# Performance work log

Measured on AMD Instinct MI355X. Metric: run time of the kernel, lower is better.

The kernel has to match this reference:

```python
import jax, jax.numpy as jnp
import numpy as np

N = 100000
H = 512
NUM_HEADS = 8
G = 512  # number of graphs (segments)


def seg_softmax(s, batch, num_segments):
    # numerically stable segment softmax (PyG-style, +1e-16 in denom)
    m = jax.ops.segment_max(s, batch, num_segments=num_segments)
    e = jnp.exp(s - m[batch])
    d = jax.ops.segment_sum(e, batch, num_segments=num_segments)
    return e / (d[batch] + 1e-16)


def setup_inputs() -> dict:
    key = jax.random.key(0)
    ks = jax.random.split(key, 12)
    s = 0.02
    x = jax.random.normal(ks[0], (N, H), dtype=jnp.float32)
    batch = jnp.sort(jax.random.randint(ks[1], (N,), 0, G)).astype(jnp.int64)
    # GlobalAttention.gate_nn: Linear(H, H//2) -> ReLU -> Linear(H//2, 1)
    ga_g_w1 = jax.random.normal(ks[2], (H, H // 2), dtype=jnp.float32) * s
    ga_g_b1 = jnp.zeros((H // 2,), dtype=jnp.float32)
    ga_g_w2 = jax.random.normal(ks[3], (H // 2, 1), dtype=jnp.float32) * s
    ga_g_b2 = jnp.zeros((1,), dtype=jnp.float32)
    # GlobalAttention.nn: Linear(H, H) -> ReLU
    ga_n_w = jax.random.normal(ks[4], (H, H), dtype=jnp.float32) * s
    ga_n_b = jnp.zeros((H,), dtype=jnp.float32)
    # outer gate_nn: Linear(H, H) -> ReLU -> (Dropout: identity in eval) -> Linear(H, NUM_HEADS)
    g_w1 = jax.random.normal(ks[5], (H, H), dtype=jnp.float32) * s
    g_b1 = jnp.zeros((H,), dtype=jnp.float32)
    g_w2 = jax.random.normal(ks[6], (H, NUM_HEADS), dtype=jnp.float32) * s
    g_b2 = jnp.zeros((NUM_HEADS,), dtype=jnp.float32)
    return dict(x=x, batch=batch,
                ga_g_w1=ga_g_w1, ga_g_b1=ga_g_b1, ga_g_w2=ga_g_w2, ga_g_b2=ga_g_b2,
                ga_n_w=ga_n_w, ga_n_b=ga_n_b,
                g_w1=g_w1, g_b1=g_b1, g_w2=g_w2, g_b2=g_b2)


def reference(x, batch, ga_g_w1, ga_g_b1, ga_g_w2, ga_g_b2, ga_n_w, ga_n_b,
              g_w1, g_b1, g_w2, g_b2):
    # --- GlobalAttention pooling ---
    h = jax.nn.relu(x @ ga_g_w1 + ga_g_b1)          # (N, H//2)
    gate = (h @ ga_g_w2 + ga_g_b2)[:, 0]            # (N,)
    gate = seg_softmax(gate, batch, G)              # segment softmax per graph
    xt = jax.nn.relu(x @ ga_n_w + ga_n_b)           # (N, H)
    graph_embedding = jax.ops.segment_sum(gate[:, None] * xt, batch,
                                          num_segments=G)  # (G, H)
    # --- interpretable attention weights ---
    g = jax.nn.relu(x @ g_w1 + g_b1)                # (N, H); dropout = identity (eval)
    scores = (g @ g_w2 + g_b2).mean(axis=-1)        # (N,) mean over heads
    attention = seg_softmax(scores, batch, G)       # (N,)
    return graph_embedding, attention
```

## Files before the change

### kernel.cpp

```cpp
#include <hip/hip_runtime.h>

#define NN 100000
#define HH 512
#define GG 512
#define NPACK 1280
#define NSTRIP 80
#define SB 16384
#define XTROWS (NN + 128)

typedef unsigned short u16;
typedef unsigned int u32;
typedef __bf16 bf16x8 __attribute__((ext_vector_type(8)));
typedef unsigned short u16x8 __attribute__((ext_vector_type(8)));
typedef float f32x4 __attribute__((ext_vector_type(4)));
typedef __attribute__((address_space(1))) void gvoid_t;
typedef __attribute__((address_space(3))) void lvoid_t;

__device__ __forceinline__ u16 f2bf(float f) {
    unsigned u = __float_as_uint(f);
    unsigned r = u + 0x7FFFu + ((u >> 16) & 1u);
    return (u16)(r >> 16);
}
__device__ __forceinline__ float bf2f(u16 b) {
    return __uint_as_float(((unsigned)b) << 16);
}

__global__ void k_prep(const float* __restrict__ gw1, const float* __restrict__ gb1,
                       const float* __restrict__ gw2v,
                       const float* __restrict__ nw, const float* __restrict__ nb,
                       const float* __restrict__ aw1, const float* __restrict__ ab1,
                       const float* __restrict__ aw2, const int* __restrict__ batch,
                       u16* __restrict__ WT, float2* __restrict__ bwv,
                       int* __restrict__ starts) {
    int idx = blockIdx.x * blockDim.x + threadIdx.x;
    int stride = gridDim.x * blockDim.x;
    for (int i = idx; i < NPACK * 512; i += stride) {
        int n = i >> 9, k = i & 511;
        float v;
        if (n < 256)      v = gw1[k * 256 + n];
        else if (n < 768) v = nw[k * 512 + (n - 256)];
        else              v = aw1[k * 512 + (n - 768)];
        int s = n >> 4, nl = n & 15;
        int ck = k >> 3, k3 = k & 7;
        size_t byte = (size_t)s * SB + nl * 1024 + ((size_t)(ck ^ nl) << 4) + k3 * 2;
        *(u16*)((char*)WT + byte) = f2bf(v);
    }
    for (int n = idx; n < NPACK; n += stride) {
        float bi, wv;
        if (n < 256)      { bi = gb1[n];       wv = gw2v[n]; }
        else if (n < 768) { bi = nb[n - 256];  wv = 0.f; }
        else {
            bi = ab1[n - 768];
            float s = 0.f;
            for (int h = 0; h < 8; ++h) s += aw2[(n - 768) * 8 + h];
            wv = s * 0.125f;
        }
        bwv[n] = make_float2(bi, wv);
    }
    for (int g = idx; g <= GG; g += stride) {
        if (g == GG) { starts[GG] = NN; continue; }
        int lo = 0, hi = NN;
        while (lo < hi) { int mid = (lo + hi) >> 1; if (batch[mid] < g) lo = mid + 1; else hi = mid; }
        starts[g] = lo;
    }
}

__global__ __launch_bounds__(256, 2)
void k_gemm(const float* __restrict__ X, const u16* __restrict__ B,
            const float2* __restrict__ bwv,
            const float* __restrict__ gb2, const float* __restrict__ ab2,
            u16* __restrict__ xt, float* __restrict__ gs, float* __restrict__ as_) {
    __shared__ __align__(16) char ldsB[2 * SB];
    __shared__ __align__(8) float2 bwv_lds[NPACK];

    const int tid = threadIdx.x;
    const int lane = tid & 63;
    const int w = tid >> 6;
    const int m0 = blockIdx.x * 128;
    const int l16 = lane & 15, kq = lane >> 4;

#define STAGE(s, bsel) do {                                                          \
    const char* _src = (const char*)B + (size_t)(s) * SB + tid * 16;                 \
    char* _dst = ldsB + (bsel) * SB + tid * 16;                                      \
    _Pragma("unroll")                                                                \
    for (int _t = 0; _t < 4; ++_t)                                                   \
        __builtin_amdgcn_global_load_lds((gvoid_t*)(_src + _t * 4096),               \
                                         (lvoid_t*)(_dst + _t * 4096), 16, 0, 0);    \
} while (0)

    STAGE(0, 0);

    for (int t = tid; t < NPACK; t += 256) bwv_lds[t] = bwv[t];

    float b2 = gb2[0];
    float bb = 0.f;
#pragma unroll
    for (int h = 0; h < 8; ++h) bb += ab2[h];
    bb *= 0.125f;

    __syncthreads();

    bf16x8 a_reg[2][16];
#pragma unroll
    for (int i = 0; i < 2; ++i) {
        int row = m0 + w * 32 + i * 16 + l16;
        if (row >= NN) row = NN - 1;
        const float* xp = X + (size_t)row * 512 + kq * 8;
#pragma unroll
        for (int kt = 0; kt < 16; ++kt) {
            float4 f0 = *(const float4*)(xp + kt * 32);
            float4 f1 = *(const float4*)(xp + kt * 32 + 4);
            u16x8 u;
            u[0] = f2bf(f0.x); u[1] = f2bf(f0.y); u[2] = f2bf(f0.z); u[3] = f2bf(f0.w);
            u[4] = f2bf(f1.x); u[5] = f2bf(f1.y); u[6] = f2bf(f1.z); u[7] = f2bf(f1.w);
            a_reg[i][kt] = __builtin_bit_cast(bf16x8, u);
        }
    }

    float s_[2][4];
#pragma unroll
    for (int i = 0; i < 2; ++i)
#pragma unroll
        for (int r = 0; r < 4; ++r) s_[i][r] = 0.f;
    u32 stash[4];

    for (int nt = 0; nt < NSTRIP; ++nt) {
        const int cur = nt & 1;
        if (nt + 1 < NSTRIP) STAGE(nt + 1, cur ^ 1);

        if (nt == NSTRIP - 1)
            asm volatile("s_waitcnt vmcnt(0)" ::: "memory");
        else if (nt >= 18 && nt <= 48 && !(nt & 1))
            asm volatile("s_waitcnt vmcnt(12)" ::: "memory");
        else
            asm volatile("s_waitcnt vmcnt(4)" ::: "memory");
        __builtin_amdgcn_s_barrier();
        __builtin_amdgcn_sched_barrier(0);

        f32x4 acc[2];
        acc[0] = {0.f, 0.f, 0.f, 0.f};
        acc[1] = {0.f, 0.f, 0.f, 0.f};

        const char* bbase = ldsB + cur * SB + l16 * 1024;
        __builtin_amdgcn_s_setprio(1);
#pragma unroll
        for (int kt = 0; kt < 16; ++kt) {
            int off = ((kt * 4 + kq) ^ l16) << 4;
            bf16x8 b0 = *(const bf16x8*)(bbase + off);
            acc[0] = __builtin_amdgcn_mfma_f32_16x16x32_bf16(a_reg[0][kt], b0, acc[0], 0, 0, 0);
            acc[1] = __builtin_amdgcn_mfma_f32_16x16x32_bf16(a_reg[1][kt], b0, acc[1], 0, 0, 0);
        }
        __builtin_amdgcn_s_setprio(0);
        __builtin_amdgcn_s_barrier();

        float2 bw = bwv_lds[nt * 16 + l16];
        if (nt < 16) {
#pragma unroll
            for (int i = 0; i < 2; ++i)
#pragma unroll
                for (int r = 0; r < 4; ++r)
                    s_[i][r] += fmaxf(acc[i][r] + bw.x, 0.f) * bw.y;
            if (nt == 15) {
#pragma unroll
                for (int i = 0; i < 2; ++i)
#pragma unroll
                    for (int r = 0; r < 4; ++r) {
                        float pg = s_[i][r];
                        pg += __shfl_xor(pg, 1); pg += __shfl_xor(pg, 2);
                        pg += __shfl_xor(pg, 4); pg += __shfl_xor(pg, 8);
                        int rg = m0 + w * 32 + i * 16 + kq * 4 + r;
                        if (l16 == 0 && rg < NN) gs[rg] = pg + b2;
                        s_[i][r] = 0.f;
                    }
            }
        } else if (nt < 48) {
            const int sx = nt - 16;
            if (!(sx & 1)) {
#pragma unroll
                for (int i = 0; i < 2; ++i)
#pragma unroll
                    for (int rp = 0; rp < 2; ++rp) {
                        u32 lo = f2bf(fmaxf(acc[i][rp * 2]     + bw.x, 0.f));
                        u32 hi = f2bf(fmaxf(acc[i][rp * 2 + 1] + bw.x, 0.f));
                        stash[i * 2 + rp] = lo | (hi << 16);
                    }
            } else {
                const int s2 = sx >> 1;
#pragma unroll
                for (int i = 0; i < 2; ++i)
#pragma unroll
                    for (int r = 0; r < 4; ++r) {
                        int rg = m0 + w * 32 + i * 16 + kq * 4 + r;
                        ushort2 st;
                        st.x = (u16)(stash[i * 2 + (r >> 1)] >> ((r & 1) * 16));
                        st.y = f2bf(fmaxf(acc[i][r] + bw.x, 0.f));
                        *(ushort2*)(xt + (size_t)rg * 512 + s2 * 32 + l16 * 2) = st;
                    }
            }
        } else {
#pragma unroll
            for (int i = 0; i < 2; ++i)
#pragma unroll
                for (int r = 0; r < 4; ++r)
                    s_[i][r] += fmaxf(acc[i][r] + bw.x, 0.f) * bw.y;
        }
    }
#undef STAGE

#pragma unroll
    for (int i = 0; i < 2; ++i)
#pragma unroll
        for (int r = 0; r < 4; ++r) {
            float pa = s_[i][r];
            pa += __shfl_xor(pa, 1); pa += __shfl_xor(pa, 2);
            pa += __shfl_xor(pa, 4); pa += __shfl_xor(pa, 8);
            int rg = m0 + w * 32 + i * 16 + kq * 4 + r;
            if (l16 == 0 && rg < NN) as_[rg] = pa + bb;
        }
}

__global__ void k_seg(const float* __restrict__ gs, const float* __restrict__ as_,
                      const int* __restrict__ starts,
                      float* __restrict__ gate, float* __restrict__ attn) {
    int g = blockIdx.x;
    int s0 = starts[g], s1 = starts[g + 1];
    int tid = threadIdx.x, lane = tid & 63, w = tid >> 6;
    __shared__ float red[8];
    float lmg = -3.0e38f, lma = -3.0e38f;
    for (int i = s0 + tid; i < s1; i += 256) {
        lmg = fmaxf(lmg, gs[i]); lma = fmaxf(lma, as_[i]);
    }
    for (int o = 32; o; o >>= 1) {
        lmg = fmaxf(lmg, __shfl_xor(lmg, o));
        lma = fmaxf(lma, __shfl_xor(lma, o));
    }
    if (lane == 0) { red[w] = lmg; red[4 + w] = lma; }
    __syncthreads();
    float Mg = fmaxf(fmaxf(red[0], red[1]), fmaxf(red[2], red[3]));
    float Ma = fmaxf(fmaxf(red[4], red[5]), fmaxf(red[6], red[7]));
    __syncthreads();
    float sgv = 0.f, sav = 0.f;
    for (int i = s0 + tid; i < s1; i += 256) {
        sgv += expf(gs[i] - Mg); sav += expf(as_[i] - Ma);
    }
    for (int o = 32; o; o >>= 1) { sgv += __shfl_xor(sgv, o); sav += __shfl_xor(sav, o); }
    if (lane == 0) { red[w] = sgv; red[4 + w] = sav; }
    __syncthreads();
    float Dg = red[0] + red[1] + red[2] + red[3] + 1e-16f;
    float Da = red[4] + red[5] + red[6] + red[7] + 1e-16f;
    for (int i = s0 + tid; i < s1; i += 256) {
        gate[i] = expf(gs[i] - Mg) / Dg;
        attn[i] = expf(as_[i] - Ma) / Da;
    }
}

__global__ __launch_bounds__(256)
void k_emb(const u16* __restrict__ xt, const float* __restrict__ gate,
           const int* __restrict__ starts, float* __restrict__ out) {
    int g = blockIdx.x;
    int s0 = starts[g], s1 = starts[g + 1];
    int c2 = threadIdx.x;
    int col0 = (c2 >> 4) * 32 + (c2 & 15);
    float a0 = 0.f, a1 = 0.f;
    int n = s0;
    for (; n + 4 <= s1; n += 4) {
        ushort2 u0 = reinterpret_cast<const ushort2*>(xt + (size_t)(n + 0) * 512)[c2];
        ushort2 u1 = reinterpret_cast<const ushort2*>(xt + (size_t)(n + 1) * 512)[c2];
        ushort2 u2 = reinterpret_cast<const ushort2*>(xt + (size_t)(n + 2) * 512)[c2];
        ushort2 u3 = reinterpret_cast<const ushort2*>(xt + (size_t)(n + 3) * 512)[c2];
        float g0 = gate[n], g1 = gate[n + 1], g2 = gate[n + 2], g3 = gate[n + 3];
        a0 += g0 * bf2f(u0.x); a1 += g0 * bf2f(u0.y);
        a0 += g1 * bf2f(u1.x); a1 += g1 * bf2f(u1.y);
        a0 += g2 * bf2f(u2.x); a1 += g2 * bf2f(u2.y);
        a0 += g3 * bf2f(u3.x); a1 += g3 * bf2f(u3.y);
    }
    for (; n < s1; ++n) {
        float gn = gate[n];
        ushort2 u = reinterpret_cast<const ushort2*>(xt + (size_t)n * 512)[c2];
        a0 += gn * bf2f(u.x);
        a1 += gn * bf2f(u.y);
    }
    out[g * 512 + col0] = a0;
    out[g * 512 + col0 + 16] = a1;
}

extern "C" void kernel_launch(void* const* d_in, const int* in_sizes, int n_in,
                              void* d_out, int out_size, void* d_ws, size_t ws_size,
                              hipStream_t stream) {
    const float* x       = (const float*)d_in[0];
    const int*   batch   = (const int*)d_in[1];
    const float* ga_g_w1 = (const float*)d_in[2];
    const float* ga_g_b1 = (const float*)d_in[3];
    const float* ga_g_w2 = (const float*)d_in[4];
    const float* ga_g_b2 = (const float*)d_in[5];
    const float* ga_n_w  = (const float*)d_in[6];
    const float* ga_n_b  = (const float*)d_in[7];
    const float* g_w1    = (const float*)d_in[8];
    const float* g_b1    = (const float*)d_in[9];
    const float* g_w2    = (const float*)d_in[10];
    const float* g_b2    = (const float*)d_in[11];

    float* out_emb = (float*)d_out;
    float* out_att = out_emb + GG * HH;

    char* p = (char*)d_ws;
    size_t off = 0;
    auto alloc = [&](size_t bytes) -> char* {
        char* q = p + off;
        off += (bytes + 255) & ~(size_t)255;
        return q;
    };
    u16*    xt    = (u16*)   alloc((size_t)XTROWS * HH * 2);
    u16*    WT    = (u16*)   alloc((size_t)NPACK * 512 * 2);
    float2* bwv   = (float2*)alloc(NPACK * 8);
    float*  gs    = (float*) alloc((size_t)NN * 4);
    float*  as_   = (float*) alloc((size_t)NN * 4);
    float*  gate  = (float*) alloc((size_t)NN * 4);
    int*    starts= (int*)   alloc((GG + 1) * 4);

    k_prep<<<2560, 256, 0, stream>>>(ga_g_w1, ga_g_b1, ga_g_w2, ga_n_w, ga_n_b,
                                     g_w1, g_b1, g_w2, batch, WT, bwv, starts);
    k_gemm<<<782, 256, 0, stream>>>(x, WT, bwv, ga_g_b2, g_b2, xt, gs, as_);
    k_seg<<<GG, 256, 0, stream>>>(gs, as_, starts, gate, out_att);
    k_emb<<<GG, 256, 0, stream>>>(xt, gate, starts, out_emb);
}
```

Baseline: 522.2 us.

## Widen GEMM strips to 32 columns, fuse seg+emb kernels, tile weight prep

The GEMM now processes 32 output columns per strip (40 strips of 32 KB) with two B fragments per k-step, which halves the barrier and loop overhead and moves the prefetch after the barrier. The xt pair-stash logic is replaced by direct stores of both halves. The segment softmax and embedding reduction are fused into one kernel, with gate values kept in LDS instead of a global gate buffer. Weight packing now goes through an LDS transpose with vector stores in 161 blocks. Together these trade more LDS per block, and possibly lower occupancy, for fewer launches and fewer synchronisation points.

```diff
diff --git a/kernel.cpp b/kernel.cpp
--- a/kernel.cpp
+++ b/kernel.cpp
@@ -4,8 +4,9 @@
 #define HH 512
 #define GG 512
 #define NPACK 1280
-#define NSTRIP 80
-#define SB 16384
+#define NSTRIP 40
+#define SB 32768
+#define SB16 16384
 #define XTROWS (NN + 128)
 
 typedef unsigned short u16;
@@ -25,43 +26,63 @@
     return __uint_as_float(((unsigned)b) << 16);
 }
 
-__global__ void k_prep(const float* __restrict__ gw1, const float* __restrict__ gb1,
-                       const float* __restrict__ gw2v,
-                       const float* __restrict__ nw, const float* __restrict__ nb,
-                       const float* __restrict__ aw1, const float* __restrict__ ab1,
-                       const float* __restrict__ aw2, const int* __restrict__ batch,
-                       u16* __restrict__ WT, float2* __restrict__ bwv,
-                       int* __restrict__ starts) {
-    int idx = blockIdx.x * blockDim.x + threadIdx.x;
-    int stride = gridDim.x * blockDim.x;
-    for (int i = idx; i < NPACK * 512; i += stride) {
-        int n = i >> 9, k = i & 511;
-        float v;
-        if (n < 256)      v = gw1[k * 256 + n];
-        else if (n < 768) v = nw[k * 512 + (n - 256)];
-        else              v = aw1[k * 512 + (n - 768)];
-        int s = n >> 4, nl = n & 15;
-        int ck = k >> 3, k3 = k & 7;
-        size_t byte = (size_t)s * SB + nl * 1024 + ((size_t)(ck ^ nl) << 4) + k3 * 2;
-        *(u16*)((char*)WT + byte) = f2bf(v);
-    }
-    for (int n = idx; n < NPACK; n += stride) {
-        float bi, wv;
-        if (n < 256)      { bi = gb1[n];       wv = gw2v[n]; }
-        else if (n < 768) { bi = nb[n - 256];  wv = 0.f; }
-        else {
-            bi = ab1[n - 768];
-            float s = 0.f;
-            for (int h = 0; h < 8; ++h) s += aw2[(n - 768) * 8 + h];
-            wv = s * 0.125f;
-        }
-        bwv[n] = make_float2(bi, wv);
-    }
-    for (int g = idx; g <= GG; g += stride) {
-        if (g == GG) { starts[GG] = NN; continue; }
-        int lo = 0, hi = NN;
-        while (lo < hi) { int mid = (lo + hi) >> 1; if (batch[mid] < g) lo = mid + 1; else hi = mid; }
-        starts[g] = lo;
+__global__ __launch_bounds__(256)
+void k_prep(const float* __restrict__ gw1, const float* __restrict__ gb1,
+            const float* __restrict__ gw2v,
+            const float* __restrict__ nw, const float* __restrict__ nbias,
+            const float* __restrict__ aw1, const float* __restrict__ ab1,
+            const float* __restrict__ aw2, const int* __restrict__ batch,
+            u16* __restrict__ WT, float2* __restrict__ bwv,
+            int* __restrict__ starts) {
+    __shared__ u16 lt[64][80];
+    const int b = blockIdx.x, tid = threadIdx.x;
+    if (b < 160) {
+        const int bn = b >> 3, bk = b & 7;
+        const int N0 = bn * 64, K0 = bk * 64;
+        const float* src; int LD, nb0;
+        if (N0 < 256)      { src = gw1; LD = 256; nb0 = N0; }
+        else if (N0 < 768) { src = nw;  LD = 512; nb0 = N0 - 256; }
+        else               { src = aw1; LD = 512; nb0 = N0 - 768; }
+        const int kr = tid >> 2, q = tid & 3;
+        const float* sp = src + (size_t)(K0 + kr) * LD + nb0 + q * 16;
+#pragma unroll
+        for (int jj = 0; jj < 4; ++jj) {
+            float4 f = *(const float4*)(sp + jj * 4);
+            lt[q * 16 + jj * 4 + 0][kr] = f2bf(f.x);
+            lt[q * 16 + jj * 4 + 1][kr] = f2bf(f.y);
+            lt[q * 16 + jj * 4 + 2][kr] = f2bf(f.z);
+            lt[q * 16 + jj * 4 + 3][kr] = f2bf(f.w);
+        }
+        __syncthreads();
+        const int nlcl = tid >> 2, c2 = tid & 3;
+        const int n = N0 + nlcl;
+        const int s = n >> 4, nl = n & 15;
+#pragma unroll
+        for (int cc = 0; cc < 2; ++cc) {
+            int c = c2 * 2 + cc;
+            int ckb = (K0 >> 3) + c;
+            size_t byte = (size_t)s * SB16 + nl * 1024 + ((size_t)(ckb ^ nl) << 4);
+            *(u16x8*)((char*)WT + byte) = *(const u16x8*)(&lt[nlcl][c * 8]);
+        }
+    } else {
+        for (int n = tid; n < NPACK; n += 256) {
+            float bi, wv;
+            if (n < 256)      { bi = gb1[n];        wv = gw2v[n]; }
+            else if (n < 768) { bi = nbias[n - 256]; wv = 0.f; }
+            else {
+                bi = ab1[n - 768];
+                float s = 0.f;
+                for (int h = 0; h < 8; ++h) s += aw2[(n - 768) * 8 + h];
+                wv = s * 0.125f;
+            }
+            bwv[n] = make_float2(bi, wv);
+        }
+        for (int g = tid; g <= GG; g += 256) {
+            if (g == GG) { starts[GG] = NN; continue; }
+            int lo = 0, hi = NN;
+            while (lo < hi) { int mid = (lo + hi) >> 1; if (batch[mid] < g) lo = mid + 1; else hi = mid; }
+            starts[g] = lo;
+        }
     }
 }
 
@@ -83,7 +104,7 @@
     const char* _src = (const char*)B + (size_t)(s) * SB + tid * 16;                 \
     char* _dst = ldsB + (bsel) * SB + tid * 16;                                      \
     _Pragma("unroll")                                                                \
-    for (int _t = 0; _t < 4; ++_t)                                                   \
+    for (int _t = 0; _t < 8; ++_t)                                                   \
         __builtin_amdgcn_global_load_lds((gvoid_t*)(_src + _t * 4096),               \
                                          (lvoid_t*)(_dst + _t * 4096), 16, 0, 0);    \
 } while (0)
@@ -97,8 +118,6 @@
 #pragma unroll
     for (int h = 0; h < 8; ++h) bb += ab2[h];
     bb *= 0.125f;
-
-    __syncthreads();
 
     bf16x8 a_reg[2][16];
 #pragma unroll
@@ -122,24 +141,22 @@
     for (int i = 0; i < 2; ++i)
 #pragma unroll
         for (int r = 0; r < 4; ++r) s_[i][r] = 0.f;
-    u32 stash[4];
+
+    __syncthreads();
 
     for (int nt = 0; nt < NSTRIP; ++nt) {
         const int cur = nt & 1;
-        if (nt + 1 < NSTRIP) STAGE(nt + 1, cur ^ 1);
-
-        if (nt == NSTRIP - 1)
-            asm volatile("s_waitcnt vmcnt(0)" ::: "memory");
-        else if (nt >= 18 && nt <= 48 && !(nt & 1))
-            asm volatile("s_waitcnt vmcnt(12)" ::: "memory");
-        else
-            asm volatile("s_waitcnt vmcnt(4)" ::: "memory");
+
+        if (nt >= 8 && nt <= 24) asm volatile("s_waitcnt vmcnt(8)" ::: "memory");
+        else                     asm volatile("s_waitcnt vmcnt(0)" ::: "memory");
         __builtin_amdgcn_s_barrier();
         __builtin_amdgcn_sched_barrier(0);
 
-        f32x4 acc[2];
-        acc[0] = {0.f, 0.f, 0.f, 0.f};
-        acc[1] = {0.f, 0.f, 0.f, 0.f};
+        if (nt + 1 < NSTRIP) STAGE(nt + 1, cur ^ 1);
+
+        f32x4 acc[2][2];
+#pragma unroll
+        for (int i = 0; i < 2; ++i) { acc[i][0] = {0.f,0.f,0.f,0.f}; acc[i][1] = {0.f,0.f,0.f,0.f}; }
 
         const char* bbase = ldsB + cur * SB + l16 * 1024;
         __builtin_amdgcn_s_setprio(1);
@@ -147,20 +164,37 @@
         for (int kt = 0; kt < 16; ++kt) {
             int off = ((kt * 4 + kq) ^ l16) << 4;
             bf16x8 b0 = *(const bf16x8*)(bbase + off);
-            acc[0] = __builtin_amdgcn_mfma_f32_16x16x32_bf16(a_reg[0][kt], b0, acc[0], 0, 0, 0);
-            acc[1] = __builtin_amdgcn_mfma_f32_16x16x32_bf16(a_reg[1][kt], b0, acc[1], 0, 0, 0);
+            bf16x8 b1 = *(const bf16x8*)(bbase + 16384 + off);
+#pragma unroll
+            for (int i = 0; i < 2; ++i) {
+                acc[i][0] = __builtin_amdgcn_mfma_f32_16x16x32_bf16(a_reg[i][kt], b0, acc[i][0], 0, 0, 0);
+                acc[i][1] = __builtin_amdgcn_mfma_f32_16x16x32_bf16(a_reg[i][kt], b1, acc[i][1], 0, 0, 0);
+            }
         }
         __builtin_amdgcn_s_setprio(0);
-        __builtin_amdgcn_s_barrier();
-
-        float2 bw = bwv_lds[nt * 16 + l16];
-        if (nt < 16) {
+
+        float2 bw0 = bwv_lds[nt * 32 + l16];
+        float2 bw1 = bwv_lds[nt * 32 + 16 + l16];
+        if (nt >= 8 && nt < 24) {
+            const int sx = nt - 8;
 #pragma unroll
             for (int i = 0; i < 2; ++i)
 #pragma unroll
+                for (int r = 0; r < 4; ++r) {
+                    int rg = m0 + w * 32 + i * 16 + kq * 4 + r;
+                    ushort2 st;
+                    st.x = f2bf(fmaxf(acc[i][0][r] + bw0.x, 0.f));
+                    st.y = f2bf(fmaxf(acc[i][1][r] + bw1.x, 0.f));
+                    *(ushort2*)(xt + (size_t)rg * 512 + sx * 32 + l16 * 2) = st;
+                }
+        } else {
+#pragma unroll
+            for (int i = 0; i < 2; ++i)
+#pragma unroll
                 for (int r = 0; r < 4; ++r)
-                    s_[i][r] += fmaxf(acc[i][r] + bw.x, 0.f) * bw.y;
-            if (nt == 15) {
+                    s_[i][r] += fmaxf(acc[i][0][r] + bw0.x, 0.f) * bw0.y
+                              + fmaxf(acc[i][1][r] + bw1.x, 0.f) * bw1.y;
+            if (nt == 7) {
 #pragma unroll
                 for (int i = 0; i < 2; ++i)
 #pragma unroll
@@ -173,36 +207,6 @@
                         s_[i][r] = 0.f;
                     }
             }
-        } else if (nt < 48) {
-            const int sx = nt - 16;
-            if (!(sx & 1)) {
-#pragma unroll
-                for (int i = 0; i < 2; ++i)
-#pragma unroll
-                    for (int rp = 0; rp < 2; ++rp) {
-                        u32 lo = f2bf(fmaxf(acc[i][rp * 2]     + bw.x, 0.f));
-                        u32 hi = f2bf(fmaxf(acc[i][rp * 2 + 1] + bw.x, 0.f));
-                        stash[i * 2 + rp] = lo | (hi << 16);
-                    }
-            } else {
-                const int s2 = sx >> 1;
-#pragma unroll
-                for (int i = 0; i < 2; ++i)
-#pragma unroll
-                    for (int r = 0; r < 4; ++r) {
-                        int rg = m0 + w * 32 + i * 16 + kq * 4 + r;
-                        ushort2 st;
-                        st.x = (u16)(stash[i * 2 + (r >> 1)] >> ((r & 1) * 16));
-                        st.y = f2bf(fmaxf(acc[i][r] + bw.x, 0.f));
-                        *(ushort2*)(xt + (size_t)rg * 512 + s2 * 32 + l16 * 2) = st;
-                    }
-            }
-        } else {
-#pragma unroll
-            for (int i = 0; i < 2; ++i)
-#pragma unroll
-                for (int r = 0; r < 4; ++r)
-                    s_[i][r] += fmaxf(acc[i][r] + bw.x, 0.f) * bw.y;
         }
     }
 #undef STAGE
@@ -219,13 +223,16 @@
         }
 }
 
-__global__ void k_seg(const float* __restrict__ gs, const float* __restrict__ as_,
-                      const int* __restrict__ starts,
-                      float* __restrict__ gate, float* __restrict__ attn) {
-    int g = blockIdx.x;
-    int s0 = starts[g], s1 = starts[g + 1];
-    int tid = threadIdx.x, lane = tid & 63, w = tid >> 6;
+__global__ __launch_bounds__(256)
+void k_post(const float* __restrict__ gs, const float* __restrict__ as_,
+            const u16* __restrict__ xt, const int* __restrict__ starts,
+            float* __restrict__ out_emb, float* __restrict__ out_att) {
+    const int g = blockIdx.x;
+    const int s0 = starts[g], s1 = starts[g + 1];
+    const int tid = threadIdx.x, lane = tid & 63, w = tid >> 6;
     __shared__ float red[8];
+    __shared__ float gbuf[1024];
+
     float lmg = -3.0e38f, lma = -3.0e38f;
     for (int i = s0 + tid; i < s1; i += 256) {
         lmg = fmaxf(lmg, gs[i]); lma = fmaxf(lma, as_[i]);
@@ -246,42 +253,42 @@
     for (int o = 32; o; o >>= 1) { sgv += __shfl_xor(sgv, o); sav += __shfl_xor(sav, o); }
     if (lane == 0) { red[w] = sgv; red[4 + w] = sav; }
     __syncthreads();
-    float Dg = red[0] + red[1] + red[2] + red[3] + 1e-16f;
-    float Da = red[4] + red[5] + red[6] + red[7] + 1e-16f;
-    for (int i = s0 + tid; i < s1; i += 256) {
-        gate[i] = expf(gs[i] - Mg) / Dg;
-        attn[i] = expf(as_[i] - Ma) / Da;
-    }
-}
-
-__global__ __launch_bounds__(256)
-void k_emb(const u16* __restrict__ xt, const float* __restrict__ gate,
-           const int* __restrict__ starts, float* __restrict__ out) {
-    int g = blockIdx.x;
-    int s0 = starts[g], s1 = starts[g + 1];
-    int c2 = threadIdx.x;
-    int col0 = (c2 >> 4) * 32 + (c2 & 15);
+    const float Dg = red[0] + red[1] + red[2] + red[3] + 1e-16f;
+    const float Da = red[4] + red[5] + red[6] + red[7] + 1e-16f;
+
+    const int c2 = tid;
+    const int col0 = (c2 >> 4) * 32 + (c2 & 15);
     float a0 = 0.f, a1 = 0.f;
-    int n = s0;
-    for (; n + 4 <= s1; n += 4) {
-        ushort2 u0 = reinterpret_cast<const ushort2*>(xt + (size_t)(n + 0) * 512)[c2];
-        ushort2 u1 = reinterpret_cast<const ushort2*>(xt + (size_t)(n + 1) * 512)[c2];
-        ushort2 u2 = reinterpret_cast<const ushort2*>(xt + (size_t)(n + 2) * 512)[c2];
-        ushort2 u3 = reinterpret_cast<const ushort2*>(xt + (size_t)(n + 3) * 512)[c2];
-        float g0 = gate[n], g1 = gate[n + 1], g2 = gate[n + 2], g3 = gate[n + 3];
-        a0 += g0 * bf2f(u0.x); a1 += g0 * bf2f(u0.y);
-        a0 += g1 * bf2f(u1.x); a1 += g1 * bf2f(u1.y);
-        a0 += g2 * bf2f(u2.x); a1 += g2 * bf2f(u2.y);
-        a0 += g3 * bf2f(u3.x); a1 += g3 * bf2f(u3.y);
-    }
-    for (; n < s1; ++n) {
-        float gn = gate[n];
-        ushort2 u = reinterpret_cast<const ushort2*>(xt + (size_t)n * 512)[c2];
-        a0 += gn * bf2f(u.x);
-        a1 += gn * bf2f(u.y);
-    }
-    out[g * 512 + col0] = a0;
-    out[g * 512 + col0 + 16] = a1;
+    for (int nb = s0; nb < s1; nb += 1024) {
+        const int ce = min(s1, nb + 1024);
+        __syncthreads();
+        for (int i = nb + tid; i < ce; i += 256) {
+            gbuf[i - nb] = expf(gs[i] - Mg) / Dg;
+            out_att[i]   = expf(as_[i] - Ma) / Da;
+        }
+        __syncthreads();
+        const int cl = ce - nb;
+        int j = 0;
+        for (; j + 4 <= cl; j += 4) {
+            const size_t n = (size_t)(nb + j);
+            ushort2 u0 = ((const ushort2*)(xt + (n + 0) * 512))[c2];
+            ushort2 u1 = ((const ushort2*)(xt + (n + 1) * 512))[c2];
+            ushort2 u2 = ((const ushort2*)(xt + (n + 2) * 512))[c2];
+            ushort2 u3 = ((const ushort2*)(xt + (n + 3) * 512))[c2];
+            float g0 = gbuf[j], g1 = gbuf[j + 1], g2 = gbuf[j + 2], g3 = gbuf[j + 3];
+            a0 += g0 * bf2f(u0.x); a1 += g0 * bf2f(u0.y);
+            a0 += g1 * bf2f(u1.x); a1 += g1 * bf2f(u1.y);
+            a0 += g2 * bf2f(u2.x); a1 += g2 * bf2f(u2.y);
+            a0 += g3 * bf2f(u3.x); a1 += g3 * bf2f(u3.y);
+        }
+        for (; j < cl; ++j) {
+            ushort2 u = ((const ushort2*)(xt + (size_t)(nb + j) * 512))[c2];
+            float gj = gbuf[j];
+            a0 += gj * bf2f(u.x); a1 += gj * bf2f(u.y);
+        }
+    }
+    out_emb[g * 512 + col0] = a0;
+    out_emb[g * 512 + col0 + 16] = a1;
 }
 
 extern "C" void kernel_launch(void* const* d_in, const int* in_sizes, int n_in,
@@ -315,12 +322,10 @@
     float2* bwv   = (float2*)alloc(NPACK * 8);
     float*  gs    = (float*) alloc((size_t)NN * 4);
     float*  as_   = (float*) alloc((size_t)NN * 4);
-    float*  gate  = (float*) alloc((size_t)NN * 4);
     int*    starts= (int*)   alloc((GG + 1) * 4);
 
-    k_prep<<<2560, 256, 0, stream>>>(ga_g_w1, ga_g_b1, ga_g_w2, ga_n_w, ga_n_b,
-                                     g_w1, g_b1, g_w2, batch, WT, bwv, starts);
+    k_prep<<<161, 256, 0, stream>>>(ga_g_w1, ga_g_b1, ga_g_w2, ga_n_w, ga_n_b,
+                                    g_w1, g_b1, g_w2, batch, WT, bwv, starts);
     k_gemm<<<782, 256, 0, stream>>>(x, WT, bwv, ga_g_b2, g_b2, xt, gs, as_);
-    k_seg<<<GG, 256, 0, stream>>>(gs, as_, starts, gate, out_att);
-    k_emb<<<GG, 256, 0, stream>>>(xt, gate, starts, out_emb);
-}
+    k_post<<<GG, 256, 0, stream>>>(gs, as_, xt, starts, out_emb, out_att);
+}
```

Result: faster. 487.0 us (-6.7%).
